# Kernel tuning notes

Measured on AMD Instinct MI355X. Metric: run time of the kernel, lower is better.

The kernel has to match this reference:

```python
import jax, jax.numpy as jnp
import numpy as np
import math
from jax import lax

B, M, T = 32, 80, 10000
EPS = 1e-6
DELTA_CLAMP = (0.001, 0.1)


def setup_inputs() -> dict:
    key = jax.random.key(0)
    k_mel, = jax.random.split(key, 1)
    # linear mel energies: non-negative
    mel = jax.random.uniform(k_mel, (B, M, T), dtype=jnp.float32)

    def full(v):
        return jnp.full((M,), v, dtype=jnp.float32)

    # exact init values from the torch module
    log_s = full(math.log(0.15 / (1 - 0.15)))
    log_alpha = full(math.log(0.99 / (1 - 0.99)))
    log_delta = full(math.log(0.01))
    log_r = full(math.log(0.1 / (1 - 0.1)))
    return {"mel": mel, "log_s": log_s, "log_alpha": log_alpha,
            "log_delta": log_delta, "log_r": log_r}


def reference(mel, log_s, log_alpha, log_delta, log_r):
    # per-channel coefficients, clamped exactly as in torch
    s = jnp.clip(jax.nn.sigmoid(log_s), 0.05, 0.3)            # (M,)
    alpha = jnp.clip(jax.nn.sigmoid(log_alpha), 0.9, 0.999)   # (M,)
    delta = jnp.clip(jnp.exp(log_delta), *DELTA_CLAMP)        # (M,)
    r = jnp.clip(jax.nn.sigmoid(log_r), 0.05, 0.25)           # (M,)

    # EMA smoother along time via scan. Torch inits smoother = mel[:,:,0]
    # and the t=0 update yields (1-s)*mel0 + s*mel0 = mel0, so we scan over
    # all T frames with init = mel[:,:,0].
    s_bm = s[None, :]                      # (1, M) broadcasts over (B, M)

    def step(smoother, x_t):
        new = (1.0 - s_bm) * smoother + s_bm * x_t
        return new, new

    xs = jnp.moveaxis(mel, -1, 0)          # (T, B, M)
    _, sm = lax.scan(step, mel[:, :, 0], xs)
    smoothed = jnp.moveaxis(sm, 0, -1)     # (B, M, T)

    alpha_c = alpha[None, :, None]
    delta_c = delta[None, :, None]
    r_c = r[None, :, None]

    gain = (EPS + smoothed) ** (-alpha_c)
    pcen = (mel * gain + delta_c) ** r_c - delta_c ** r_c
    return pcen
```

## Files before the change

kernel.cpp:

```cpp
#include <hip/hip_runtime.h>
#include <math.h>


constexpr int B_ = 32, M_ = 80, T_ = 10000;
constexpr int EPI   = 256;
constexpr int CHUNK = 2048;
constexpr int NCH   = (T_ + CHUNK - 1) / CHUNK;
constexpr int ITERS = CHUNK / EPI;
constexpr float EPS_ = 1e-6f;

__device__ __forceinline__ float pcen_one(float x, float y, float alpha,
                                          float delta, float r, float dr) {
    float g = __expf(-alpha * __logf(y + EPS_));
    float z = fmaf(x, g, delta);
    return __expf(r * __logf(z)) - dr;
}

struct ScanCoef {
    float s, a, a2, a3, a4;
    float c0, c1, c2, c3, c4, c5;
    float a4lane;
};

__device__ __forceinline__ float scan256(float4 x, const ScanCoef& k, int lane,
                                         float yprev,
                                         float& y0, float& y1, float& y2, float& y3) {
    float l0 = k.s * x.x;
    float l1 = fmaf(k.a, l0, k.s * x.y);
    float l2 = fmaf(k.a, l1, k.s * x.z);
    float l3 = fmaf(k.a, l2, k.s * x.w);

    float S = l3, t;
    t = __shfl_up(S, 1);  if (lane >= 1)  S = fmaf(k.c0, t, S);
    t = __shfl_up(S, 2);  if (lane >= 2)  S = fmaf(k.c1, t, S);
    t = __shfl_up(S, 4);  if (lane >= 4)  S = fmaf(k.c2, t, S);
    t = __shfl_up(S, 8);  if (lane >= 8)  S = fmaf(k.c3, t, S);
    t = __shfl_up(S, 16); if (lane >= 16) S = fmaf(k.c4, t, S);
    t = __shfl_up(S, 32); if (lane >= 32) S = fmaf(k.c5, t, S);

    float Sp = __shfl_up(S, 1);
    float C  = fmaf(k.a4lane, yprev, (lane == 0) ? 0.0f : Sp);

    y0 = fmaf(k.a,  C, l0);
    y1 = fmaf(k.a2, C, l1);
    y2 = fmaf(k.a3, C, l2);
    y3 = fmaf(k.a4, C, l3);

    float S63 = __shfl(S, 63);
    float a256 = k.c5 * k.c5;
    return fmaf(a256, yprev, S63);
}

__global__ __launch_bounds__(256) void pcen_kernel(
    const float* __restrict__ mel,
    const float* __restrict__ log_s,
    const float* __restrict__ log_alpha,
    const float* __restrict__ log_delta,
    const float* __restrict__ log_r,
    float* __restrict__ out)
{
    const int lane = threadIdx.x & 63;
    const int wv   = threadIdx.x >> 6;
    const int gw   = blockIdx.x * 4 + wv;
    if (gw >= B_ * M_ * NCH) return;
    const int row = gw / NCH;
    const int c   = gw % NCH;
    const int m   = row % M_;

    float s = 1.0f / (1.0f + __expf(-log_s[m]));
    s = fminf(fmaxf(s, 0.05f), 0.3f);
    float alpha = 1.0f / (1.0f + __expf(-log_alpha[m]));
    alpha = fminf(fmaxf(alpha, 0.9f), 0.999f);
    float delta = __expf(log_delta[m]);
    delta = fminf(fmaxf(delta, 0.001f), 0.1f);
    float r = 1.0f / (1.0f + __expf(-log_r[m]));
    r = fminf(fmaxf(r, 0.05f), 0.25f);
    const float dr = __expf(r * __logf(delta));

    ScanCoef k;
    k.s = s; k.a = 1.0f - s;
    k.a2 = k.a * k.a; k.a3 = k.a2 * k.a; k.a4 = k.a2 * k.a2;
    k.c0 = k.a4; k.c1 = k.c0 * k.c0; k.c2 = k.c1 * k.c1;
    k.c3 = k.c2 * k.c2; k.c4 = k.c3 * k.c3; k.c5 = k.c4 * k.c4;
    k.a4lane = __expf(__logf(k.a) * (float)(4 * lane));

    const size_t rb   = (size_t)row * T_;
    const float* mp   = mel + rb;
    float*       op   = out + rb;
    const int    start = c * CHUNK;

    float yprev;
    float y0, y1, y2, y3;

    if (c == 0) {
        float4 xh = *(const float4*)(mp + lane * 4);
        yprev = __shfl(xh.x, 0);
    } else {
        float4 xh = *(const float4*)(mp + (start - EPI) + lane * 4);
        yprev = __shfl(xh.x, 0);
        yprev = scan256(xh, k, lane, yprev, y0, y1, y2, y3);
    }

    int base = start + lane * 4;
    bool act = base < T_;
    float4 x = act ? *(const float4*)(mp + base)
                   : make_float4(0.f, 0.f, 0.f, 0.f);

    for (int it = 0; it < ITERS; ++it) {
        int   base_n = base + EPI;
        bool  act_n  = (it + 1 < ITERS) && (base_n < T_);
        float4 xn = act_n ? *(const float4*)(mp + base_n)
                          : make_float4(0.f, 0.f, 0.f, 0.f);

        yprev = scan256(x, k, lane, yprev, y0, y1, y2, y3);

        if (act) {
            float4 o;
            o.x = pcen_one(x.x, y0, alpha, delta, r, dr);
            o.y = pcen_one(x.y, y1, alpha, delta, r, dr);
            o.z = pcen_one(x.z, y2, alpha, delta, r, dr);
            o.w = pcen_one(x.w, y3, alpha, delta, r, dr);
            *(float4*)(op + base) = o;
        }

        x = xn; base = base_n; act = act_n;
    }
}

extern "C" void kernel_launch(void* const* d_in, const int* in_sizes, int n_in,
                              void* d_out, int out_size, void* d_ws, size_t ws_size,
                              hipStream_t stream) {
    const float* mel       = (const float*)d_in[0];
    const float* log_s     = (const float*)d_in[1];
    const float* log_alpha = (const float*)d_in[2];
    const float* log_delta = (const float*)d_in[3];
    const float* log_r     = (const float*)d_in[4];
    float* out = (float*)d_out;

    const int nwaves = B_ * M_ * NCH;
    dim3 grid((nwaves + 3) / 4);
    pcen_kernel<<<grid, 256, 0, stream>>>(mel, log_s, log_alpha, log_delta,
                                          log_r, out);
}
```

Baseline: 196.6 us.

## Scan 8 elements per lane and software-pipeline the next block's scan

Each lane now handles 8 consecutive time steps per iteration (512 per wave step), which halves the number of shuffle-based wave scans per chunk. The local prefix and shuffle scan for the next block run before the pcen output of the current block, so the dependent shuffle chain overlaps with transcendental work. Lane-conditional branches are folded into precomputed zeroed coefficients, and broadcasts use readlane. The cost is more registers per thread and a possible out-of-bounds read of the first block when the last chunk starts near the end of the row.

```diff
diff --git a/kernel.cpp b/kernel.cpp
--- a/kernel.cpp
+++ b/kernel.cpp
@@ -3,52 +3,14 @@
 
 
 constexpr int B_ = 32, M_ = 80, T_ = 10000;
-constexpr int EPI   = 256;
+constexpr int EPI   = 512;
 constexpr int CHUNK = 2048;
 constexpr int NCH   = (T_ + CHUNK - 1) / CHUNK;
 constexpr int ITERS = CHUNK / EPI;
 constexpr float EPS_ = 1e-6f;
 
-__device__ __forceinline__ float pcen_one(float x, float y, float alpha,
-                                          float delta, float r, float dr) {
-    float g = __expf(-alpha * __logf(y + EPS_));
-    float z = fmaf(x, g, delta);
-    return __expf(r * __logf(z)) - dr;
-}
-
-struct ScanCoef {
-    float s, a, a2, a3, a4;
-    float c0, c1, c2, c3, c4, c5;
-    float a4lane;
-};
-
-__device__ __forceinline__ float scan256(float4 x, const ScanCoef& k, int lane,
-                                         float yprev,
-                                         float& y0, float& y1, float& y2, float& y3) {
-    float l0 = k.s * x.x;
-    float l1 = fmaf(k.a, l0, k.s * x.y);
-    float l2 = fmaf(k.a, l1, k.s * x.z);
-    float l3 = fmaf(k.a, l2, k.s * x.w);
-
-    float S = l3, t;
-    t = __shfl_up(S, 1);  if (lane >= 1)  S = fmaf(k.c0, t, S);
-    t = __shfl_up(S, 2);  if (lane >= 2)  S = fmaf(k.c1, t, S);
-    t = __shfl_up(S, 4);  if (lane >= 4)  S = fmaf(k.c2, t, S);
-    t = __shfl_up(S, 8);  if (lane >= 8)  S = fmaf(k.c3, t, S);
-    t = __shfl_up(S, 16); if (lane >= 16) S = fmaf(k.c4, t, S);
-    t = __shfl_up(S, 32); if (lane >= 32) S = fmaf(k.c5, t, S);
-
-    float Sp = __shfl_up(S, 1);
-    float C  = fmaf(k.a4lane, yprev, (lane == 0) ? 0.0f : Sp);
-
-    y0 = fmaf(k.a,  C, l0);
-    y1 = fmaf(k.a2, C, l1);
-    y2 = fmaf(k.a3, C, l2);
-    y3 = fmaf(k.a4, C, l3);
-
-    float S63 = __shfl(S, 63);
-    float a256 = k.c5 * k.c5;
-    return fmaf(a256, yprev, S63);
+__device__ __forceinline__ float bcastlane(float v, int l) {
+    return __int_as_float(__builtin_amdgcn_readlane(__float_as_int(v), l));
 }
 
 __global__ __launch_bounds__(256) void pcen_kernel(
@@ -67,64 +29,109 @@
     const int c   = gw % NCH;
     const int m   = row % M_;
 
-    float s = 1.0f / (1.0f + __expf(-log_s[m]));
-    s = fminf(fmaxf(s, 0.05f), 0.3f);
-    float alpha = 1.0f / (1.0f + __expf(-log_alpha[m]));
-    alpha = fminf(fmaxf(alpha, 0.9f), 0.999f);
-    float delta = __expf(log_delta[m]);
-    delta = fminf(fmaxf(delta, 0.001f), 0.1f);
-    float r = 1.0f / (1.0f + __expf(-log_r[m]));
-    r = fminf(fmaxf(r, 0.05f), 0.25f);
+    float s = 1.f / (1.f + __expf(-log_s[m]));         s = fminf(fmaxf(s, 0.05f), 0.3f);
+    float alpha = 1.f / (1.f + __expf(-log_alpha[m])); alpha = fminf(fmaxf(alpha, 0.9f), 0.999f);
+    float delta = __expf(log_delta[m]);                delta = fminf(fmaxf(delta, 0.001f), 0.1f);
+    float r = 1.f / (1.f + __expf(-log_r[m]));         r = fminf(fmaxf(r, 0.05f), 0.25f);
     const float dr = __expf(r * __logf(delta));
 
-    ScanCoef k;
-    k.s = s; k.a = 1.0f - s;
-    k.a2 = k.a * k.a; k.a3 = k.a2 * k.a; k.a4 = k.a2 * k.a2;
-    k.c0 = k.a4; k.c1 = k.c0 * k.c0; k.c2 = k.c1 * k.c1;
-    k.c3 = k.c2 * k.c2; k.c4 = k.c3 * k.c3; k.c5 = k.c4 * k.c4;
-    k.a4lane = __expf(__logf(k.a) * (float)(4 * lane));
+    const float a  = 1.f - s;
+    const float a2 = a*a,  a3 = a2*a,  a4 = a2*a2,
+                a5 = a4*a, a6 = a4*a2, a7 = a4*a3, a8 = a4*a4;
+    const float a16 = a8*a8, a32 = a16*a16, a64 = a32*a32,
+                a128 = a64*a64, a256 = a128*a128, a512 = a256*a256;
+    const float k1  = (lane >= 1 ) ? a8   : 0.f;
+    const float k2  = (lane >= 2 ) ? a16  : 0.f;
+    const float k4  = (lane >= 4 ) ? a32  : 0.f;
+    const float k8  = (lane >= 8 ) ? a64  : 0.f;
+    const float k16 = (lane >= 16) ? a128 : 0.f;
+    const float k32 = (lane >= 32) ? a256 : 0.f;
+    const float a8lane = __expf(__logf(a) * (float)(8 * lane));
 
-    const size_t rb   = (size_t)row * T_;
-    const float* mp   = mel + rb;
-    float*       op   = out + rb;
-    const int    start = c * CHUNK;
+    const float* mp = mel + (size_t)row * T_;
+    float*       op = out + (size_t)row * T_;
+    const int start = c * CHUNK;
+
+    auto scanA = [&](float4 xa, float4 xb, float* l) -> float {
+        l[0] = s * xa.x;
+        l[1] = fmaf(a, l[0], s * xa.y);
+        l[2] = fmaf(a, l[1], s * xa.z);
+        l[3] = fmaf(a, l[2], s * xa.w);
+        l[4] = fmaf(a, l[3], s * xb.x);
+        l[5] = fmaf(a, l[4], s * xb.y);
+        l[6] = fmaf(a, l[5], s * xb.z);
+        l[7] = fmaf(a, l[6], s * xb.w);
+        float S = l[7], t;
+        t = __shfl_up(S, 1);  S = fmaf(k1,  t, S);
+        t = __shfl_up(S, 2);  S = fmaf(k2,  t, S);
+        t = __shfl_up(S, 4);  S = fmaf(k4,  t, S);
+        t = __shfl_up(S, 8);  S = fmaf(k8,  t, S);
+        t = __shfl_up(S, 16); S = fmaf(k16, t, S);
+        t = __shfl_up(S, 32); S = fmaf(k32, t, S);
+        return S;
+    };
+    auto pcen1 = [&](float x, float y) {
+        float g = __expf(-alpha * __logf(y + EPS_));
+        float z = fmaf(x, g, delta);
+        return __expf(r * __logf(z)) - dr;
+    };
+
+    int base = start + lane * 8;
+    float4 xa = *(const float4*)(mp + base);
+    float4 xb = *(const float4*)(mp + base + 4);
+    float l[8];
+    float S = scanA(xa, xb, l);
 
     float yprev;
-    float y0, y1, y2, y3;
-
     if (c == 0) {
-        float4 xh = *(const float4*)(mp + lane * 4);
-        yprev = __shfl(xh.x, 0);
+        yprev = bcastlane(xa.x, 0);
     } else {
-        float4 xh = *(const float4*)(mp + (start - EPI) + lane * 4);
-        yprev = __shfl(xh.x, 0);
-        yprev = scan256(xh, k, lane, yprev, y0, y1, y2, y3);
+        const float* hp = mp + (start - EPI) + lane * 8;
+        float4 ha = *(const float4*)(hp);
+        float4 hb = *(const float4*)(hp + 4);
+        float hl[8];
+        float hS = scanA(ha, hb, hl);
+        yprev = fmaf(a512, bcastlane(ha.x, 0), bcastlane(hS, 63));
     }
 
-    int base = start + lane * 4;
-    bool act = base < T_;
-    float4 x = act ? *(const float4*)(mp + base)
-                   : make_float4(0.f, 0.f, 0.f, 0.f);
+    auto doB = [&](const float4& Xa, const float4& Xb, const float* L,
+                   float Sv, int bas) {
+        float Sp = __shfl_up(Sv, 1);
+        float C  = fmaf(a8lane, yprev, (lane == 0) ? 0.f : Sp);
+        yprev = fmaf(a512, yprev, bcastlane(Sv, 63));
+        if (bas < T_) {
+            float4 o1, o2;
+            o1.x = pcen1(Xa.x, fmaf(a,  C, L[0]));
+            o1.y = pcen1(Xa.y, fmaf(a2, C, L[1]));
+            o1.z = pcen1(Xa.z, fmaf(a3, C, L[2]));
+            o1.w = pcen1(Xa.w, fmaf(a4, C, L[3]));
+            o2.x = pcen1(Xb.x, fmaf(a5, C, L[4]));
+            o2.y = pcen1(Xb.y, fmaf(a6, C, L[5]));
+            o2.z = pcen1(Xb.z, fmaf(a7, C, L[6]));
+            o2.w = pcen1(Xb.w, fmaf(a8, C, L[7]));
+            *(float4*)(op + bas)     = o1;
+            *(float4*)(op + bas + 4) = o2;
+        }
+    };
 
-    for (int it = 0; it < ITERS; ++it) {
-        int   base_n = base + EPI;
-        bool  act_n  = (it + 1 < ITERS) && (base_n < T_);
-        float4 xn = act_n ? *(const float4*)(mp + base_n)
-                          : make_float4(0.f, 0.f, 0.f, 0.f);
-
-        yprev = scan256(x, k, lane, yprev, y0, y1, y2, y3);
-
-        if (act) {
-            float4 o;
-            o.x = pcen_one(x.x, y0, alpha, delta, r, dr);
-            o.y = pcen_one(x.y, y1, alpha, delta, r, dr);
-            o.z = pcen_one(x.z, y2, alpha, delta, r, dr);
-            o.w = pcen_one(x.w, y3, alpha, delta, r, dr);
-            *(float4*)(op + base) = o;
+    #pragma unroll
+    for (int it = 0; it < ITERS - 1; ++it) {
+        const int base_n = base + EPI;
+        const bool act_n = base_n < T_;
+        float4 xan = make_float4(0.f, 0.f, 0.f, 0.f), xbn = xan;
+        if (act_n) {
+            xan = *(const float4*)(mp + base_n);
+            xbn = *(const float4*)(mp + base_n + 4);
         }
-
-        x = xn; base = base_n; act = act_n;
+        float ln[8];
+        float Sn = scanA(xan, xbn, ln);
+        doB(xa, xb, l, S, base);
+        xa = xan; xb = xbn; S = Sn;
+        #pragma unroll
+        for (int j = 0; j < 8; ++j) l[j] = ln[j];
+        base = base_n;
     }
+    doB(xa, xb, l, S, base);
 }
 
 extern "C" void kernel_launch(void* const* d_in, const int* in_sizes, int n_in,
```

Result: no change. 194.8 us (-0.9%).
